# Kernel optimization log

Hardware: AMD Instinct MI355X
Metric: run time of the kernel (lower is better)

The kernel has to match this reference:

```python
import jax, jax.numpy as jnp
import numpy as np

SEL = 20   # selection_length
NN2 = 10   # org_dim*num_library_fns % SEL
NN3 = 22   # org_dim*num_library_fns // SEL - NN2


def _all_combos(L):
    # all 2^L binary vectors of length L; equals union over popcounts of
    # set(itertools.permutations([1]*c + [0]*(L-c))) in the torch code
    ints = jnp.arange(2 ** L, dtype=jnp.uint32)
    bits = (ints[:, None] >> jnp.arange(L, dtype=jnp.uint32)[None, :]) & jnp.uint32(1)
    return bits.astype(jnp.float32)  # [2^L, L]


def _chunk_step(params, combos, combo_sums, prob, chunk):
    """Replicates Model._compute_selarr_output_grad for one chunk.
    params: (W1 [H,L+1], b1 [H], W2 [1,H], b2 [1]) of net2 or net3.
    combos: [N, L] all binary vectors; combo_sums: [N] int popcounts.
    prob: scalar carry probability; chunk: [L] the actual selection.
    """
    W1, b1, W2, b2 = params
    N = combos.shape[0]
    x_all = jnp.concatenate([jnp.full((N, 1), prob, combos.dtype), combos], axis=1)  # [N, L+1]
    h = jnp.tanh(x_all @ W1.T + b1)          # [N, H]
    out = h @ W2[0] + b2[0]                  # [N]
    choices = jnp.round(jnp.sum(chunk)).astype(jnp.int32)
    mask = (combo_sums == choices).astype(combos.dtype)  # valid combinations only
    output_sum = jnp.sum(mask * jnp.exp(out))
    # grad_sum = sum_j out_j * d out_j / d theta (masked), closed form:
    w = mask * out
    s = (1.0 - h * h) * W2[0]                # [N, H]
    gs_W1 = jnp.einsum('n,nh,nd->hd', w, s, x_all)
    gs_b1 = jnp.einsum('n,nh->h', w, s)
    gs_W2 = jnp.einsum('n,nh->h', w, h)[None, :]
    gs_b2 = jnp.sum(w)[None]
    # the key combination = the actual chunk
    xk = jnp.concatenate([prob[None], chunk])
    hk = jnp.tanh(W1 @ xk + b1)
    outk = W2[0] @ hk + b2[0]
    sk = (1.0 - hk * hk) * W2[0]
    p_out = jnp.exp(outk) / output_sum
    grads = (jnp.outer(sk, xk) - gs_W1 / output_sum,
             sk - gs_b1 / output_sum,
             hk[None, :] - gs_W2 / output_sum,
             jnp.ones((1,), xk.dtype) - gs_b2 / output_sum)
    return p_out, grads


def _run_group(params, chunks, prob0):
    L = chunks.shape[1]
    combos = _all_combos(L)
    combo_sums = jnp.round(jnp.sum(combos, axis=1)).astype(jnp.int32)

    def step(carry, chunk):
        prob, acc = carry
        p, g = _chunk_step(params, combos, combo_sums, prob, chunk)
        acc = tuple(a + gi for a, gi in zip(acc, g))
        return (p, acc), p

    acc0 = tuple(jnp.zeros_like(p) for p in params)
    (prob_f, acc), ps = jax.lax.scan(step, (prob0, acc0), chunks)
    return prob_f, acc, ps


def setup_inputs() -> dict:
    key = jax.random.key(0)
    ks = jax.random.split(key, 10)
    total = NN2 * (SEL + 1) + NN3 * SEL  # 650
    selection_arr = jax.random.bernoulli(ks[0], 0.5, (total,)).astype(jnp.float32)
    p0 = jax.random.uniform(ks[1], (1,), jnp.float32)

    def lin(kw, kb, fan_out, fan_in):
        bound = 1.0 / np.sqrt(fan_in)
        W = jax.random.uniform(kw, (fan_out, fan_in), jnp.float32, -bound, bound)
        b = jax.random.uniform(kb, (fan_out,), jnp.float32, -bound, bound)
        return W, b

    W1_2, b1_2 = lin(ks[2], ks[3], 4, SEL + 2)  # net2: Linear(sel+2, 4)
    W2_2, b2_2 = lin(ks[4], ks[5], 1, 4)
    W1_3, b1_3 = lin(ks[6], ks[7], 4, SEL + 1)  # net3: Linear(sel+1, 4)
    W2_3, b2_3 = lin(ks[8], ks[9], 1, 4)
    return {'probability_lib_selection': p0, 'selection_arr': selection_arr,
            'W1_2': W1_2, 'b1_2': b1_2, 'W2_2': W2_2, 'b2_2': b2_2,
            'W1_3': W1_3, 'b1_3': b1_3, 'W2_3': W2_3, 'b2_3': b2_3}


def reference(probability_lib_selection, selection_arr,
              W1_2, b1_2, W2_2, b2_2, W1_3, b1_3, W2_3, b2_3):
    p0 = probability_lib_selection[0]
    n2 = NN2 * (SEL + 1)
    chunks2 = selection_arr[:n2].reshape(NN2, SEL + 1)
    chunks3 = selection_arr[n2:n2 + NN3 * SEL].reshape(NN3, SEL)
    p_after2, g2, ps2 = _run_group((W1_2, b1_2, W2_2, b2_2), chunks2, p0)
    _, g3, ps3 = _run_group((W1_3, b1_3, W2_3, b2_3), chunks3, p_after2)
    sample_probability_array = jnp.concatenate([p0[None], ps2, ps3])  # [1+NN2+NN3]
    return (sample_probability_array,) + g2 + g3
```

## Files before the change

### kernel.cpp

```cpp
#include <hip/hip_runtime.h>
#include <cstdint>
#include <cmath>

#define DEV __device__ __forceinline__

constexpr int SEL = 20;
constexpr int NSTEP2 = 10, NSTEP3 = 22, NSTEPS = 32;
constexpr int L2 = SEL + 1;
constexpr int L3 = SEL;
constexpr int FBE = 7;
constexpr int FBS2 = L2 - FBE;
constexpr int FBS3 = L3 - FBE;
constexpr int BT = 128;

typedef float v2f __attribute__((ext_vector_type(2)));

constexpr float K2E = 2.8853900817779268f;
constexpr float KE  = 1.4426950408889634f;

struct Binom { unsigned v[22][22]; };
constexpr Binom make_binom() {
  Binom b{};
  for (int n = 0; n < 22; n++) {
    b.v[n][0] = 1;
    for (int k = 1; k < 22; k++)
      b.v[n][k] = (k > n) ? 0u : (k == n ? 1u : b.v[n - 1][k - 1] + b.v[n - 1][k]);
  }
  return b;
}
constexpr Binom BN_H = make_binom();
__device__ constexpr Binom BN = make_binom();

constexpr unsigned ceil64u(unsigned x) { return (x + 63u) & ~63u; }
constexpr int padded_count(int NB) {
  int s = 0;
  for (int k = 0; k <= NB; k++) s += (int)ceil64u(BN_H.v[NB][k]);
  return s;
}
constexpr int NPAT2P = padded_count(FBS2);
constexpr int NPAT3P = padded_count(FBS3);

constexpr int SUMS_STRIDE = 96;
constexpr int OFF_SUMS   = 0;
constexpr int OFF_KEYB   = OFF_SUMS + NSTEPS * SUMS_STRIDE;
constexpr int OFF_CT     = OFF_KEYB + 128;
constexpr int OFF_CB     = OFF_CT + 32;
constexpr int OFF_REP    = OFF_CB + 32;
constexpr int OFF_ZEND   = OFF_REP + 32;
constexpr int OFF_PAT2   = OFF_ZEND;
constexpr int OFF_PAT3   = OFF_PAT2 + NPAT2P;

DEV float fast_tanh(float x) {
  float e = exp2f(x * K2E);
  return 1.0f - 2.0f * __builtin_amdgcn_rcpf(e + 1.0f);
}
DEV float fast_exp(float x) { return exp2f(x * KE); }
DEV void gatomic(float* p, float v) { unsafeAtomicAdd(p, v); }

DEV unsigned gosper(unsigned cmb) {
  unsigned u = cmb & (~cmb + 1u);
  unsigned v = cmb + u;
  return v | ((cmb ^ v) >> (1 + __ffs(u)));
}

DEV float dppsum64(float x) {
  float f = x;
  f += __int_as_float(__builtin_amdgcn_update_dpp(0, __float_as_int(f), 0x111, 0xf, 0xf, false));
  f += __int_as_float(__builtin_amdgcn_update_dpp(0, __float_as_int(f), 0x112, 0xf, 0xf, false));
  f += __int_as_float(__builtin_amdgcn_update_dpp(0, __float_as_int(f), 0x114, 0xf, 0xf, false));
  f += __int_as_float(__builtin_amdgcn_update_dpp(0, __float_as_int(f), 0x118, 0xf, 0xf, false));
  f += __int_as_float(__builtin_amdgcn_update_dpp(0, __float_as_int(f), 0x142, 0xa, 0xf, false));
  f += __int_as_float(__builtin_amdgcn_update_dpp(0, __float_as_int(f), 0x143, 0xc, 0xf, false));
  return f;
}

__global__ void kz(const float* p0, const float* sel,
                   const float* W1_2, const float* b1_2,
                   const float* W1_3, const float* b1_3, float* ws) {
  int tx = threadIdx.x;
  if (blockIdx.x == 0) {
    __shared__ int sc[NSTEPS];
    for (int i = tx; i < OFF_ZEND; i += blockDim.x) ws[i] = 0.0f;
    __syncthreads();
    if (tx < NSTEPS) {
      int t = tx;
      int g = (t < NSTEP2) ? 0 : 1;
      int L = g ? L3 : L2;
      const float* sbase = sel + (g ? (NSTEP2 * L2 + (t - NSTEP2) * L3) : t * L2);
      unsigned cb = 0; int c = 0;
      for (int d = 0; d < L; d++)
        if (sbase[d] > 0.5f) { cb |= 1u << d; c++; }
      sc[t] = c;
      ((int*)ws)[OFF_CT + t] = c;
      ((unsigned*)ws)[OFF_CB + t] = cb;
      const float* W1 = g ? W1_3 : W1_2;
      const float* b1 = g ? b1_3 : b1_2;
      for (int h = 0; h < 4; h++) {
        float s = b1[h];
        for (int d = 0; d < L; d++)
          if ((cb >> d) & 1) s += W1[h * (L + 1) + 1 + d];
        ws[OFF_KEYB + t * 4 + h] = s;
      }
    }
    __syncthreads();
    if (tx < NSTEPS) {
      int r = tx;
      int start = (tx == 0) ? 0 : ((tx < NSTEP2) ? 1 : NSTEP2);
      for (int u = start; u < tx; u++)
        if (sc[u] == sc[tx]) { r = u; break; }
      ((int*)ws)[OFF_REP + tx] = r;
    }
  } else {
    int r = (blockIdx.x - 1) * 256 + tx;
    if (r >= NPAT2P + NPAT3P) return;
    int NB, rr, off;
    if (r < NPAT2P) { NB = FBS2; rr = r; off = OFF_PAT2; }
    else            { NB = FBS3; rr = r - NPAT2P; off = OFF_PAT3; }
    unsigned pat = 0xFFFFFFFFu;
    unsigned base = 0;
    for (int kk = 0; kk <= NB; kk++) {
      unsigned csz = BN.v[NB][kk];
      unsigned psz = (csz + 63u) & ~63u;
      if ((unsigned)rr < base + psz) {
        unsigned local = (unsigned)rr - base;
        if (local < csz) {
          unsigned p2 = 0; int k2 = kk;
          for (int bb = NB - 1; bb >= 0 && k2 > 0; bb--) {
            unsigned cnt = BN.v[bb][k2];
            if (local >= cnt) { p2 |= 1u << bb; local -= cnt; k2--; }
          }
          pat = p2;
        }
        break;
      }
      base += psz;
    }
    ((unsigned*)ws)[off + rr] = pat;
  }
}

template<int LL>
DEV void build_tabs(const float* W1, float4 add,
                    float4* tabEX, float4* tabS0, float4* tabS1) {
  constexpr int NS1 = 1 << (LL - 14);
  int tx = threadIdx.x;
  for (int i = tx; i < 256 + NS1; i += BT) {
    if (i < 128) {
      int e = i;
      float s0 = 0, s1 = 0, s2 = 0, s3 = 0;
      for (int j = 0; j < 7; j++) if ((e >> j) & 1) {
        s0 += W1[0 * (LL + 1) + 1 + j]; s1 += W1[1 * (LL + 1) + 1 + j];
        s2 += W1[2 * (LL + 1) + 1 + j]; s3 += W1[3 * (LL + 1) + 1 + j];
      }
      tabEX[e] = make_float4(exp2f(K2E * s0), exp2f(K2E * s1), exp2f(K2E * s2), exp2f(K2E * s3));
    } else if (i < 256) {
      int e = i - 128;
      float s0 = add.x, s1 = add.y, s2 = add.z, s3 = add.w;
      for (int j = 0; j < 7; j++) if ((e >> j) & 1) {
        s0 += W1[0 * (LL + 1) + 1 + 7 + j]; s1 += W1[1 * (LL + 1) + 1 + 7 + j];
        s2 += W1[2 * (LL + 1) + 1 + 7 + j]; s3 += W1[3 * (LL + 1) + 1 + 7 + j];
      }
      tabS0[e] = make_float4(s0, s1, s2, s3);
    } else {
      int e = i - 256;
      float s0 = 0, s1 = 0, s2 = 0, s3 = 0;
      for (int j = 0; j < LL - 14; j++) if ((e >> j) & 1) {
        s0 += W1[0 * (LL + 1) + 1 + 14 + j]; s1 += W1[1 * (LL + 1) + 1 + 14 + j];
        s2 += W1[2 * (LL + 1) + 1 + 14 + j]; s3 += W1[3 * (LL + 1) + 1 + 14 + j];
      }
      tabS1[e] = make_float4(s0, s1, s2, s3);
    }
  }
}

constexpr int KC_B2 = NPAT2P / BT;
constexpr int KC_B3 = NPAT3P / BT;
constexpr int KC_BLOCKS = NSTEP2 * KC_B2 + NSTEP3 * KC_B3;

template<int LL>
DEV void kc_work(int t, int sub, float pval,
                 const float* W1, const float* b1, const float* W2, const float* b2,
                 float* ws, float4* tabEX, float4* tabS0, float4* tabS1, float* sS) {
  constexpr int FS = LL - FBE;
  constexpr int NS1M = (1 << (LL - 14)) - 1;
  int tx = threadIdx.x;
  int c = ((const int*)ws)[OFF_CT + t];
  const unsigned* pats = ((const unsigned*)ws) + (LL == 21 ? OFF_PAT2 : OFF_PAT3);
  int pcF = __popc(pats[sub * BT]);
  int pcL = __popc(pats[sub * BT + 64]);
  if (c < pcF || c - pcL > FBE) return;
  float4 add = make_float4(b1[0] + pval * W1[0 * (LL + 1)], b1[1] + pval * W1[1 * (LL + 1)],
                           b1[2] + pval * W1[2 * (LL + 1)], b1[3] + pval * W1[3 * (LL + 1)]);
  build_tabs<LL>(W1, add, tabEX, tabS0, tabS1);
  if (tx < SUMS_STRIDE) sS[tx] = 0.0f;
  __syncthreads();
  unsigned pat = pats[sub * BT + tx];
  int ce = c - __popc(pat);
  int ce_s = __builtin_amdgcn_readfirstlane(ce);
  int trip = (ce_s >= 0 && ce_s <= FBE) ? (int)BN.v[FBE][ce_s] : 0;
  if (trip > 0) {
    float valid = (ce == ce_s) ? 1.0f : 0.0f;
    float4 vS0 = tabS0[pat & 127];
    float4 vS1 = tabS1[(pat >> 7) & NS1M];
    float E0 = exp2f(K2E * (vS0.x + vS1.x));
    float E1 = exp2f(K2E * (vS0.y + vS1.y));
    float E2 = exp2f(K2E * (vS0.z + vS1.z));
    float E3 = exp2f(K2E * (vS0.w + vS1.w));
    float w0 = W2[0], w1 = W2[1], w2 = W2[2], w3 = W2[3];
    float W0 = b2[0] + w0 + w1 + w2 + w3;
    float m0 = -2.0f * w0, m1 = -2.0f * w1, m2 = -2.0f * w2, m3 = -2.0f * w3;
    float M0 = 4.0f * w0, M1 = 4.0f * w1, M2 = 4.0f * w2, M3 = 4.0f * w3;

    float aE = 0.0f, aW = 0.0f;
    v2f aQa = {0, 0}, aQb = {0, 0}, ORa = {0, 0}, ORb = {0, 0};
#define G_DECL(k) v2f g##k##a = {0, 0}, g##k##b = {0, 0};
    G_DECL(0) G_DECL(1) G_DECL(2) G_DECL(3) G_DECL(4) G_DECL(5) G_DECL(6)
#undef G_DECL

    unsigned ivs = (1u << ce_s) - 1u;
    float4 tE = tabEX[ivs & 127];
#pragma unroll 1
    for (int k = 0; k < trip; k++) {
      float4 cur = tE;
      unsigned ivc = ivs;
      ivs = gosper(ivs);
      tE = tabEX[ivs & 127];
      float r0 = __builtin_amdgcn_rcpf(fmaf(cur.x, E0, 1.0f));
      float r1 = __builtin_amdgcn_rcpf(fmaf(cur.y, E1, 1.0f));
      float r2 = __builtin_amdgcn_rcpf(fmaf(cur.z, E2, 1.0f));
      float r3 = __builtin_amdgcn_rcpf(fmaf(cur.w, E3, 1.0f));
      float outv = W0;
      outv = fmaf(m0, r0, outv); outv = fmaf(m1, r1, outv);
      outv = fmaf(m2, r2, outv); outv = fmaf(m3, r3, outv);
      float e = exp2f(KE * outv) * valid;
      outv *= valid;
      float u0 = fmaf(-r0, r0, r0), u1 = fmaf(-r1, r1, r1);
      float u2 = fmaf(-r2, r2, r2), u3 = fmaf(-r3, r3, r3);
      float q0 = outv * (M0 * u0), q1 = outv * (M1 * u1);
      float q2 = outv * (M2 * u2), q3 = outv * (M3 * u3);
      v2f qa = {q0, q1}, qb = {q2, q3};
      aE += e; aW += outv;
      aQa += qa; aQb += qb;
      ORa += (v2f){outv * r0, outv * r1};
      ORb += (v2f){outv * r2, outv * r3};
#define G_UPD(k) if (ivc & (1u << k)) { g##k##a += qa; g##k##b += qb; }
      G_UPD(0) G_UPD(1) G_UPD(2) G_UPD(3) G_UPD(4) G_UPD(5) G_UPD(6)
#undef G_UPD
    }
    v2f aWHa = {aW - 2.0f * ORa.x, aW - 2.0f * ORa.y};
    v2f aWHb = {aW - 2.0f * ORb.x, aW - 2.0f * ORb.y};

    int lane = tx & 63;
    float rr;
    rr = dppsum64(aE); if (lane == 63 && rr != 0.0f) atomicAdd(&sS[0], rr);
    rr = dppsum64(aW); if (lane == 63 && rr != 0.0f) atomicAdd(&sS[1], rr);
    rr = dppsum64(aQa.x); if (lane == 63 && rr != 0.0f) atomicAdd(&sS[2], rr);
    rr = dppsum64(aQa.y); if (lane == 63 && rr != 0.0f) atomicAdd(&sS[3], rr);
    rr = dppsum64(aQb.x); if (lane == 63 && rr != 0.0f) atomicAdd(&sS[4], rr);
    rr = dppsum64(aQb.y); if (lane == 63 && rr != 0.0f) atomicAdd(&sS[5], rr);
    rr = dppsum64(aWHa.x); if (lane == 63 && rr != 0.0f) atomicAdd(&sS[6], rr);
    rr = dppsum64(aWHa.y); if (lane == 63 && rr != 0.0f) atomicAdd(&sS[7], rr);
    rr = dppsum64(aWHb.x); if (lane == 63 && rr != 0.0f) atomicAdd(&sS[8], rr);
    rr = dppsum64(aWHb.y); if (lane == 63 && rr != 0.0f) atomicAdd(&sS[9], rr);
#define GF(k) { \
    rr = dppsum64(g##k##a.x); if (lane == 63 && rr != 0.0f) atomicAdd(&sS[10 + 0 * 21 + k], rr); \
    rr = dppsum64(g##k##a.y); if (lane == 63 && rr != 0.0f) atomicAdd(&sS[10 + 1 * 21 + k], rr); \
    rr = dppsum64(g##k##b.x); if (lane == 63 && rr != 0.0f) atomicAdd(&sS[10 + 2 * 21 + k], rr); \
    rr = dppsum64(g##k##b.y); if (lane == 63 && rr != 0.0f) atomicAdd(&sS[10 + 3 * 21 + k], rr); }
    GF(0) GF(1) GF(2) GF(3) GF(4) GF(5) GF(6)
#undef GF
#pragma unroll
    for (int j = 0; j < 14; j++) {
      if (j < FS) {
        float m = (float)((pat >> j) & 1u);
        rr = dppsum64(m * aQa.x); if (lane == 63 && rr != 0.0f) atomicAdd(&sS[10 + 0 * 21 + FBE + j], rr);
        rr = dppsum64(m * aQa.y); if (lane == 63 && rr != 0.0f) atomicAdd(&sS[10 + 1 * 21 + FBE + j], rr);
        rr = dppsum64(m * aQb.x); if (lane == 63 && rr != 0.0f) atomicAdd(&sS[10 + 2 * 21 + FBE + j], rr);
        rr = dppsum64(m * aQb.y); if (lane == 63 && rr != 0.0f) atomicAdd(&sS[10 + 3 * 21 + FBE + j], rr);
      }
    }
  }
  __syncthreads();
  if (tx < SUMS_STRIDE) {
    float v = sS[tx];
    if (v != 0.0f) gatomic(&ws[OFF_SUMS + t * SUMS_STRIDE + tx], v);
  }
}

__global__ __launch_bounds__(BT) void kc(
    const float* p0,
    const float* W1_2, const float* b1_2, const float* W2_2, const float* b2_2,
    const float* W1_3, const float* b1_3, const float* W2_3, const float* b2_3,
    float* ws) {
  __shared__ float4 tabEX[128], tabS0[128], tabS1[128];
  __shared__ float sS[SUMS_STRIDE];
  int b = blockIdx.x;
  int t, sub;
  if (b < NSTEP2 * KC_B2) { t = b / KC_B2; sub = b % KC_B2; }
  else { int b3 = b - NSTEP2 * KC_B2; t = NSTEP2 + b3 / KC_B3; sub = b3 % KC_B3; }
  int rep = ((const int*)ws)[OFF_REP + t];
  if (rep != t) return;
  float pval = (t == 0) ? p0[0] : 0.0f;
  if (t < NSTEP2) kc_work<21>(t, sub, pval, W1_2, b1_2, W2_2, b2_2, ws, tabEX, tabS0, tabS1, sS);
  else            kc_work<20>(t, sub, pval, W1_3, b1_3, W2_3, b2_3, ws, tabEX, tabS0, tabS1, sS);
}

__global__ __launch_bounds__(256) void kd(const float* p0in,
                   const float* W1_2, const float* b1_2, const float* W2_2, const float* b2_2,
                   const float* W1_3, const float* b1_3, const float* W2_3, const float* b2_3,
                   const float* ws, float* out) {
  __shared__ float sS[NSTEPS * SUMS_STRIDE];
  __shared__ float sKEYB[128];
  __shared__ float sk_s[NSTEPS][4], hk_s[NSTEPS][4], pp_s[NSTEPS], s0i_s[NSTEPS];
  __shared__ int sREP[NSTEPS];
  int tx = threadIdx.x;
  for (int i = tx; i < NSTEPS * SUMS_STRIDE; i += 256) sS[i] = ws[OFF_SUMS + i];
  for (int i = tx; i < 128; i += 256) sKEYB[i] = ws[OFF_KEYB + i];
  if (tx < NSTEPS) sREP[tx] = ((const int*)ws)[OFF_REP + tx];
  __syncthreads();
  if (tx == 0) {
    float p = p0in[0];
    out[0] = p;
    for (int t = 0; t < NSTEPS; t++) {
      int g = (t < NSTEP2) ? 0 : 1;
      int L = g ? L3 : L2;
      const float* W1 = g ? W1_3 : W1_2;
      const float* W2 = g ? W2_3 : W2_2;
      float b2s = (g ? b2_3 : b2_2)[0];
      pp_s[t] = p;
      float outk = b2s;
      for (int h = 0; h < 4; h++)
        outk += W2[h] * fast_tanh(sKEYB[t * 4 + h] + p * W1[h * (L + 1)]);
      float Se = sS[sREP[t] * SUMS_STRIDE + 0];
      p = fast_exp(outk) / Se;
      out[1 + t] = p;
    }
  }
  __syncthreads();
  if (tx < NSTEPS) {
    int t = tx; int g = (t < NSTEP2) ? 0 : 1; int L = g ? L3 : L2;
    const float* W1 = g ? W1_3 : W1_2;
    const float* W2 = g ? W2_3 : W2_2;
    float p = pp_s[t];
    s0i_s[t] = 1.0f / sS[sREP[t] * SUMS_STRIDE + 0];
    for (int h = 0; h < 4; h++) {
      float hk = fast_tanh(sKEYB[t * 4 + h] + p * W1[h * (L + 1)]);
      hk_s[t][h] = hk;
      sk_s[t][h] = (1.0f - hk * hk) * W2[h];
    }
  }
  __syncthreads();
  const unsigned* cbp = (const unsigned*)ws;
  for (int o = 33 + tx; o < 223; o += blockDim.x) {
    float val = 0.0f;
    if (o < 130) {
      if (o < 121) {
        int e = o - 33; int h = e / 22, d = e % 22;
        for (int t = 0; t < NSTEP2; t++) {
          int rp = sREP[t];
          float xk = (d == 0) ? pp_s[t] : (float)((cbp[OFF_CB + t] >> (d - 1)) & 1);
          float gs = (d == 0) ? pp_s[t] * sS[rp * SUMS_STRIDE + 2 + h]
                              : sS[rp * SUMS_STRIDE + 10 + h * 21 + (d - 1)];
          val += sk_s[t][h] * xk - gs * s0i_s[t];
        }
      } else if (o < 125) { int h = o - 121;
        for (int t = 0; t < NSTEP2; t++) val += sk_s[t][h] - sS[sREP[t] * SUMS_STRIDE + 2 + h] * s0i_s[t];
      } else if (o < 129) { int h = o - 125;
        for (int t = 0; t < NSTEP2; t++) val += hk_s[t][h] - sS[sREP[t] * SUMS_STRIDE + 6 + h] * s0i_s[t];
      } else {
        for (int t = 0; t < NSTEP2; t++) val += 1.0f - sS[sREP[t] * SUMS_STRIDE + 1] * s0i_s[t];
      }
    } else {
      if (o < 214) {
        int e = o - 130; int h = e / 21, d = e % 21;
        for (int t = NSTEP2; t < NSTEPS; t++) {
          int rp = sREP[t];
          float xk = (d == 0) ? pp_s[t] : (float)((cbp[OFF_CB + t] >> (d - 1)) & 1);
          float gs = (d == 0) ? pp_s[t] * sS[rp * SUMS_STRIDE + 2 + h]
                              : sS[rp * SUMS_STRIDE + 10 + h * 21 + (d - 1)];
          val += sk_s[t][h] * xk - gs * s0i_s[t];
        }
      } else if (o < 218) { int h = o - 214;
        for (int t = NSTEP2; t < NSTEPS; t++) val += sk_s[t][h] - sS[sREP[t] * SUMS_STRIDE + 2 + h] * s0i_s[t];
      } else if (o < 222) { int h = o - 218;
        for (int t = NSTEP2; t < NSTEPS; t++) val += hk_s[t][h] - sS[sREP[t] * SUMS_STRIDE + 6 + h] * s0i_s[t];
      } else {
        for (int t = NSTEP2; t < NSTEPS; t++) val += 1.0f - sS[sREP[t] * SUMS_STRIDE + 1] * s0i_s[t];
      }
    }
    out[o] = val;
  }
}

extern "C" void kernel_launch(void* const* d_in, const int* in_sizes, int n_in,
                              void* d_out, int out_size, void* d_ws, size_t ws_size,
                              hipStream_t stream) {
  const float* p0   = (const float*)d_in[0];
  const float* sel  = (const float*)d_in[1];
  const float* W1_2 = (const float*)d_in[2]; const float* b1_2 = (const float*)d_in[3];
  const float* W2_2 = (const float*)d_in[4]; const float* b2_2 = (const float*)d_in[5];
  const float* W1_3 = (const float*)d_in[6]; const float* b1_3 = (const float*)d_in[7];
  const float* W2_3 = (const float*)d_in[8]; const float* b2_3 = (const float*)d_in[9];
  float* out = (float*)d_out;
  float* ws  = (float*)d_ws;
  hipLaunchKernelGGL(kz, dim3(1 + (NPAT2P + NPAT3P + 255) / 256), dim3(256), 0, stream,
                     p0, sel, W1_2, b1_2, W1_3, b1_3, ws);
  hipLaunchKernelGGL(kc, dim3(KC_BLOCKS), dim3(BT), 0, stream, p0,
                     W1_2, b1_2, W2_2, b2_2, W1_3, b1_3, W2_3, b2_3, ws);
  hipLaunchKernelGGL(kd, dim3(1), dim3(256), 0, stream, p0,
                     W1_2, b1_2, W2_2, b2_2, W1_3, b1_3, W2_3, b2_3, ws, out);
}
```

Baseline: 72.39 us.

## Precompute lookup tables once in setup kernel and use single-wave blocks

Per-block construction of the three lookup tables from W1 is moved into three dedicated blocks of the setup kernel, which write them to workspace once for each weight set (net2 with p0, net2 without, net3). The main kernel then only copies the tables into shared memory. Block size drops from 128 to 64 threads so each block is one wave, and per-block shared-memory reduction is replaced by direct global atomics from each wave. This removes redundant table building and block-level syncs, at the cost of more blocks, more global atomics, and one extra table read from global memory per block.

```diff
diff --git a/kernel.cpp b/kernel.cpp
--- a/kernel.cpp
+++ b/kernel.cpp
@@ -11,7 +11,7 @@
 constexpr int FBE = 7;
 constexpr int FBS2 = L2 - FBE;
 constexpr int FBS3 = L3 - FBE;
-constexpr int BT = 128;
+constexpr int BT = 64;
 
 typedef float v2f __attribute__((ext_vector_type(2)));
 
@@ -47,7 +47,8 @@
 constexpr int OFF_CB     = OFF_CT + 32;
 constexpr int OFF_REP    = OFF_CB + 32;
 constexpr int OFF_ZEND   = OFF_REP + 32;
-constexpr int OFF_PAT2   = OFF_ZEND;
+constexpr int OFF_TABS   = OFF_ZEND;
+constexpr int OFF_PAT2   = OFF_TABS + 3 * 384 * 4;
 constexpr int OFF_PAT3   = OFF_PAT2 + NPAT2P;
 
 DEV float fast_tanh(float x) {
@@ -78,7 +79,8 @@
                    const float* W1_2, const float* b1_2,
                    const float* W1_3, const float* b1_3, float* ws) {
   int tx = threadIdx.x;
-  if (blockIdx.x == 0) {
+  int b = blockIdx.x;
+  if (b == 0) {
     __shared__ int sc[NSTEPS];
     for (int i = tx; i < OFF_ZEND; i += blockDim.x) ws[i] = 0.0f;
     __syncthreads();
@@ -110,8 +112,43 @@
         if (sc[u] == sc[tx]) { r = u; break; }
       ((int*)ws)[OFF_REP + tx] = r;
     }
+  } else if (b <= 3) {
+    int set = b - 1;
+    int LL = (set < 2) ? L2 : L3;
+    const float* W1 = (set < 2) ? W1_2 : W1_3;
+    const float* b1 = (set < 2) ? b1_2 : b1_3;
+    float pval = (set == 0) ? p0[0] : 0.0f;
+    int NS1 = 1 << (LL - 14);
+    float4* gt = (float4*)(ws + OFF_TABS) + set * 384;
+    for (int i = tx; i < 256 + NS1; i += 256) {
+      float4 v;
+      float* vp = (float*)&v;
+      if (i < 128) {
+        int e = i;
+        for (int h = 0; h < 4; h++) {
+          float s = 0;
+          for (int j = 0; j < 7; j++) if ((e >> j) & 1) s += W1[h * (LL + 1) + 1 + j];
+          vp[h] = exp2f(K2E * s);
+        }
+      } else if (i < 256) {
+        int e = i - 128;
+        for (int h = 0; h < 4; h++) {
+          float s = b1[h] + pval * W1[h * (LL + 1)];
+          for (int j = 0; j < 7; j++) if ((e >> j) & 1) s += W1[h * (LL + 1) + 1 + 7 + j];
+          vp[h] = s;
+        }
+      } else {
+        int e = i - 256;
+        for (int h = 0; h < 4; h++) {
+          float s = 0;
+          for (int j = 0; j < LL - 14; j++) if ((e >> j) & 1) s += W1[h * (LL + 1) + 1 + 14 + j];
+          vp[h] = s;
+        }
+      }
+      gt[i] = v;
+    }
   } else {
-    int r = (blockIdx.x - 1) * 256 + tx;
+    int r = (b - 4) * 256 + tx;
     if (r >= NPAT2P + NPAT3P) return;
     int NB, rr, off;
     if (r < NPAT2P) { NB = FBS2; rr = r; off = OFF_PAT2; }
@@ -139,170 +176,132 @@
   }
 }
 
-template<int LL>
-DEV void build_tabs(const float* W1, float4 add,
-                    float4* tabEX, float4* tabS0, float4* tabS1) {
-  constexpr int NS1 = 1 << (LL - 14);
-  int tx = threadIdx.x;
-  for (int i = tx; i < 256 + NS1; i += BT) {
-    if (i < 128) {
-      int e = i;
-      float s0 = 0, s1 = 0, s2 = 0, s3 = 0;
-      for (int j = 0; j < 7; j++) if ((e >> j) & 1) {
-        s0 += W1[0 * (LL + 1) + 1 + j]; s1 += W1[1 * (LL + 1) + 1 + j];
-        s2 += W1[2 * (LL + 1) + 1 + j]; s3 += W1[3 * (LL + 1) + 1 + j];
-      }
-      tabEX[e] = make_float4(exp2f(K2E * s0), exp2f(K2E * s1), exp2f(K2E * s2), exp2f(K2E * s3));
-    } else if (i < 256) {
-      int e = i - 128;
-      float s0 = add.x, s1 = add.y, s2 = add.z, s3 = add.w;
-      for (int j = 0; j < 7; j++) if ((e >> j) & 1) {
-        s0 += W1[0 * (LL + 1) + 1 + 7 + j]; s1 += W1[1 * (LL + 1) + 1 + 7 + j];
-        s2 += W1[2 * (LL + 1) + 1 + 7 + j]; s3 += W1[3 * (LL + 1) + 1 + 7 + j];
-      }
-      tabS0[e] = make_float4(s0, s1, s2, s3);
-    } else {
-      int e = i - 256;
-      float s0 = 0, s1 = 0, s2 = 0, s3 = 0;
-      for (int j = 0; j < LL - 14; j++) if ((e >> j) & 1) {
-        s0 += W1[0 * (LL + 1) + 1 + 14 + j]; s1 += W1[1 * (LL + 1) + 1 + 14 + j];
-        s2 += W1[2 * (LL + 1) + 1 + 14 + j]; s3 += W1[3 * (LL + 1) + 1 + 14 + j];
-      }
-      tabS1[e] = make_float4(s0, s1, s2, s3);
-    }
-  }
-}
-
 constexpr int KC_B2 = NPAT2P / BT;
 constexpr int KC_B3 = NPAT3P / BT;
 constexpr int KC_BLOCKS = NSTEP2 * KC_B2 + NSTEP3 * KC_B3;
 
 template<int LL>
-DEV void kc_work(int t, int sub, float pval,
-                 const float* W1, const float* b1, const float* W2, const float* b2,
-                 float* ws, float4* tabEX, float4* tabS0, float4* tabS1, float* sS) {
+DEV void kc_work(int t, int sub, int set,
+                 const float* W2, const float* b2,
+                 float* ws, float4* tabL) {
   constexpr int FS = LL - FBE;
-  constexpr int NS1M = (1 << (LL - 14)) - 1;
+  constexpr int NS1 = 1 << (LL - 14);
+  constexpr int NS1M = NS1 - 1;
   int tx = threadIdx.x;
   int c = ((const int*)ws)[OFF_CT + t];
   const unsigned* pats = ((const unsigned*)ws) + (LL == 21 ? OFF_PAT2 : OFF_PAT3);
-  int pcF = __popc(pats[sub * BT]);
-  int pcL = __popc(pats[sub * BT + 64]);
-  if (c < pcF || c - pcL > FBE) return;
-  float4 add = make_float4(b1[0] + pval * W1[0 * (LL + 1)], b1[1] + pval * W1[1 * (LL + 1)],
-                           b1[2] + pval * W1[2 * (LL + 1)], b1[3] + pval * W1[3 * (LL + 1)]);
-  build_tabs<LL>(W1, add, tabEX, tabS0, tabS1);
-  if (tx < SUMS_STRIDE) sS[tx] = 0.0f;
-  __syncthreads();
   unsigned pat = pats[sub * BT + tx];
   int ce = c - __popc(pat);
   int ce_s = __builtin_amdgcn_readfirstlane(ce);
-  int trip = (ce_s >= 0 && ce_s <= FBE) ? (int)BN.v[FBE][ce_s] : 0;
-  if (trip > 0) {
-    float valid = (ce == ce_s) ? 1.0f : 0.0f;
-    float4 vS0 = tabS0[pat & 127];
-    float4 vS1 = tabS1[(pat >> 7) & NS1M];
-    float E0 = exp2f(K2E * (vS0.x + vS1.x));
-    float E1 = exp2f(K2E * (vS0.y + vS1.y));
-    float E2 = exp2f(K2E * (vS0.z + vS1.z));
-    float E3 = exp2f(K2E * (vS0.w + vS1.w));
-    float w0 = W2[0], w1 = W2[1], w2 = W2[2], w3 = W2[3];
-    float W0 = b2[0] + w0 + w1 + w2 + w3;
-    float m0 = -2.0f * w0, m1 = -2.0f * w1, m2 = -2.0f * w2, m3 = -2.0f * w3;
-    float M0 = 4.0f * w0, M1 = 4.0f * w1, M2 = 4.0f * w2, M3 = 4.0f * w3;
-
-    float aE = 0.0f, aW = 0.0f;
-    v2f aQa = {0, 0}, aQb = {0, 0}, ORa = {0, 0}, ORb = {0, 0};
+  if (ce_s < 0 || ce_s > FBE) return;
+  int trip = (int)BN.v[FBE][ce_s];
+  const float4* gt = (const float4*)(ws + OFF_TABS) + set * 384;
+  for (int i = tx; i < 256 + NS1; i += BT) tabL[i] = gt[i];
+  __syncthreads();
+  const float4* tabEX = tabL;
+  const float4* tabS0 = tabL + 128;
+  const float4* tabS1 = tabL + 256;
+
+  float valid = (ce == ce_s) ? 1.0f : 0.0f;
+  float4 vS0 = tabS0[pat & 127];
+  float4 vS1 = tabS1[(pat >> 7) & NS1M];
+  float E0 = exp2f(K2E * (vS0.x + vS1.x));
+  float E1 = exp2f(K2E * (vS0.y + vS1.y));
+  float E2 = exp2f(K2E * (vS0.z + vS1.z));
+  float E3 = exp2f(K2E * (vS0.w + vS1.w));
+  float w0 = W2[0], w1 = W2[1], w2 = W2[2], w3 = W2[3];
+  float W0 = b2[0] + w0 + w1 + w2 + w3;
+  float m0 = -2.0f * w0, m1 = -2.0f * w1, m2 = -2.0f * w2, m3 = -2.0f * w3;
+  float M0 = 4.0f * w0, M1 = 4.0f * w1, M2 = 4.0f * w2, M3 = 4.0f * w3;
+
+  float aE = 0.0f, aW = 0.0f;
+  v2f aQa = {0, 0}, aQb = {0, 0}, ORa = {0, 0}, ORb = {0, 0};
 #define G_DECL(k) v2f g##k##a = {0, 0}, g##k##b = {0, 0};
-    G_DECL(0) G_DECL(1) G_DECL(2) G_DECL(3) G_DECL(4) G_DECL(5) G_DECL(6)
+  G_DECL(0) G_DECL(1) G_DECL(2) G_DECL(3) G_DECL(4) G_DECL(5) G_DECL(6)
 #undef G_DECL
 
-    unsigned ivs = (1u << ce_s) - 1u;
-    float4 tE = tabEX[ivs & 127];
+  unsigned ivs = (1u << ce_s) - 1u;
+  float4 tE = tabEX[ivs & 127];
 #pragma unroll 1
-    for (int k = 0; k < trip; k++) {
-      float4 cur = tE;
-      unsigned ivc = ivs;
-      ivs = gosper(ivs);
-      tE = tabEX[ivs & 127];
-      float r0 = __builtin_amdgcn_rcpf(fmaf(cur.x, E0, 1.0f));
-      float r1 = __builtin_amdgcn_rcpf(fmaf(cur.y, E1, 1.0f));
-      float r2 = __builtin_amdgcn_rcpf(fmaf(cur.z, E2, 1.0f));
-      float r3 = __builtin_amdgcn_rcpf(fmaf(cur.w, E3, 1.0f));
-      float outv = W0;
-      outv = fmaf(m0, r0, outv); outv = fmaf(m1, r1, outv);
-      outv = fmaf(m2, r2, outv); outv = fmaf(m3, r3, outv);
-      float e = exp2f(KE * outv) * valid;
-      outv *= valid;
-      float u0 = fmaf(-r0, r0, r0), u1 = fmaf(-r1, r1, r1);
-      float u2 = fmaf(-r2, r2, r2), u3 = fmaf(-r3, r3, r3);
-      float q0 = outv * (M0 * u0), q1 = outv * (M1 * u1);
-      float q2 = outv * (M2 * u2), q3 = outv * (M3 * u3);
-      v2f qa = {q0, q1}, qb = {q2, q3};
-      aE += e; aW += outv;
-      aQa += qa; aQb += qb;
-      ORa += (v2f){outv * r0, outv * r1};
-      ORb += (v2f){outv * r2, outv * r3};
+  for (int k = 0; k < trip; k++) {
+    float4 cur = tE;
+    unsigned ivc = ivs;
+    ivs = gosper(ivs);
+    tE = tabEX[ivs & 127];
+    float r0 = __builtin_amdgcn_rcpf(fmaf(cur.x, E0, 1.0f));
+    float r1 = __builtin_amdgcn_rcpf(fmaf(cur.y, E1, 1.0f));
+    float r2 = __builtin_amdgcn_rcpf(fmaf(cur.z, E2, 1.0f));
+    float r3 = __builtin_amdgcn_rcpf(fmaf(cur.w, E3, 1.0f));
+    float outv = W0;
+    outv = fmaf(m0, r0, outv); outv = fmaf(m1, r1, outv);
+    outv = fmaf(m2, r2, outv); outv = fmaf(m3, r3, outv);
+    float e = exp2f(KE * outv) * valid;
+    outv *= valid;
+    float u0 = fmaf(-r0, r0, r0), u1 = fmaf(-r1, r1, r1);
+    float u2 = fmaf(-r2, r2, r2), u3 = fmaf(-r3, r3, r3);
+    float q0 = outv * (M0 * u0), q1 = outv * (M1 * u1);
+    float q2 = outv * (M2 * u2), q3 = outv * (M3 * u3);
+    v2f qa = {q0, q1}, qb = {q2, q3};
+    aE += e; aW += outv;
+    aQa += qa; aQb += qb;
+    ORa += (v2f){outv * r0, outv * r1};
+    ORb += (v2f){outv * r2, outv * r3};
 #define G_UPD(k) if (ivc & (1u << k)) { g##k##a += qa; g##k##b += qb; }
-      G_UPD(0) G_UPD(1) G_UPD(2) G_UPD(3) G_UPD(4) G_UPD(5) G_UPD(6)
+    G_UPD(0) G_UPD(1) G_UPD(2) G_UPD(3) G_UPD(4) G_UPD(5) G_UPD(6)
 #undef G_UPD
-    }
-    v2f aWHa = {aW - 2.0f * ORa.x, aW - 2.0f * ORa.y};
-    v2f aWHb = {aW - 2.0f * ORb.x, aW - 2.0f * ORb.y};
-
-    int lane = tx & 63;
-    float rr;
-    rr = dppsum64(aE); if (lane == 63 && rr != 0.0f) atomicAdd(&sS[0], rr);
-    rr = dppsum64(aW); if (lane == 63 && rr != 0.0f) atomicAdd(&sS[1], rr);
-    rr = dppsum64(aQa.x); if (lane == 63 && rr != 0.0f) atomicAdd(&sS[2], rr);
-    rr = dppsum64(aQa.y); if (lane == 63 && rr != 0.0f) atomicAdd(&sS[3], rr);
-    rr = dppsum64(aQb.x); if (lane == 63 && rr != 0.0f) atomicAdd(&sS[4], rr);
-    rr = dppsum64(aQb.y); if (lane == 63 && rr != 0.0f) atomicAdd(&sS[5], rr);
-    rr = dppsum64(aWHa.x); if (lane == 63 && rr != 0.0f) atomicAdd(&sS[6], rr);
-    rr = dppsum64(aWHa.y); if (lane == 63 && rr != 0.0f) atomicAdd(&sS[7], rr);
-    rr = dppsum64(aWHb.x); if (lane == 63 && rr != 0.0f) atomicAdd(&sS[8], rr);
-    rr = dppsum64(aWHb.y); if (lane == 63 && rr != 0.0f) atomicAdd(&sS[9], rr);
+  }
+  v2f aWHa = {aW - 2.0f * ORa.x, aW - 2.0f * ORa.y};
+  v2f aWHb = {aW - 2.0f * ORb.x, aW - 2.0f * ORb.y};
+
+  float* S = &ws[OFF_SUMS + t * SUMS_STRIDE];
+  int lane = tx;
+  float rr;
+  rr = dppsum64(aE); if (lane == 63 && rr != 0.0f) gatomic(&S[0], rr);
+  rr = dppsum64(aW); if (lane == 63 && rr != 0.0f) gatomic(&S[1], rr);
+  rr = dppsum64(aQa.x); if (lane == 63 && rr != 0.0f) gatomic(&S[2], rr);
+  rr = dppsum64(aQa.y); if (lane == 63 && rr != 0.0f) gatomic(&S[3], rr);
+  rr = dppsum64(aQb.x); if (lane == 63 && rr != 0.0f) gatomic(&S[4], rr);
+  rr = dppsum64(aQb.y); if (lane == 63 && rr != 0.0f) gatomic(&S[5], rr);
+  rr = dppsum64(aWHa.x); if (lane == 63 && rr != 0.0f) gatomic(&S[6], rr);
+  rr = dppsum64(aWHa.y); if (lane == 63 && rr != 0.0f) gatomic(&S[7], rr);
+  rr = dppsum64(aWHb.x); if (lane == 63 && rr != 0.0f) gatomic(&S[8], rr);
+  rr = dppsum64(aWHb.y); if (lane == 63 && rr != 0.0f) gatomic(&S[9], rr);
 #define GF(k) { \
-    rr = dppsum64(g##k##a.x); if (lane == 63 && rr != 0.0f) atomicAdd(&sS[10 + 0 * 21 + k], rr); \
-    rr = dppsum64(g##k##a.y); if (lane == 63 && rr != 0.0f) atomicAdd(&sS[10 + 1 * 21 + k], rr); \
-    rr = dppsum64(g##k##b.x); if (lane == 63 && rr != 0.0f) atomicAdd(&sS[10 + 2 * 21 + k], rr); \
-    rr = dppsum64(g##k##b.y); if (lane == 63 && rr != 0.0f) atomicAdd(&sS[10 + 3 * 21 + k], rr); }
-    GF(0) GF(1) GF(2) GF(3) GF(4) GF(5) GF(6)
+  rr = dppsum64(g##k##a.x); if (lane == 63 && rr != 0.0f) gatomic(&S[10 + 0 * 21 + k], rr); \
+  rr = dppsum64(g##k##a.y); if (lane == 63 && rr != 0.0f) gatomic(&S[10 + 1 * 21 + k], rr); \
+  rr = dppsum64(g##k##b.x); if (lane == 63 && rr != 0.0f) gatomic(&S[10 + 2 * 21 + k], rr); \
+  rr = dppsum64(g##k##b.y); if (lane == 63 && rr != 0.0f) gatomic(&S[10 + 3 * 21 + k], rr); }
+  GF(0) GF(1) GF(2) GF(3) GF(4) GF(5) GF(6)
 #undef GF
 #pragma unroll
-    for (int j = 0; j < 14; j++) {
-      if (j < FS) {
-        float m = (float)((pat >> j) & 1u);
-        rr = dppsum64(m * aQa.x); if (lane == 63 && rr != 0.0f) atomicAdd(&sS[10 + 0 * 21 + FBE + j], rr);
-        rr = dppsum64(m * aQa.y); if (lane == 63 && rr != 0.0f) atomicAdd(&sS[10 + 1 * 21 + FBE + j], rr);
-        rr = dppsum64(m * aQb.x); if (lane == 63 && rr != 0.0f) atomicAdd(&sS[10 + 2 * 21 + FBE + j], rr);
-        rr = dppsum64(m * aQb.y); if (lane == 63 && rr != 0.0f) atomicAdd(&sS[10 + 3 * 21 + FBE + j], rr);
-      }
-    }
-  }
-  __syncthreads();
-  if (tx < SUMS_STRIDE) {
-    float v = sS[tx];
-    if (v != 0.0f) gatomic(&ws[OFF_SUMS + t * SUMS_STRIDE + tx], v);
+  for (int j = 0; j < 14; j++) {
+    if (j < FS) {
+      float m = (float)((pat >> j) & 1u);
+      rr = dppsum64(m * aQa.x); if (lane == 63 && rr != 0.0f) gatomic(&S[10 + 0 * 21 + FBE + j], rr);
+      rr = dppsum64(m * aQa.y); if (lane == 63 && rr != 0.0f) gatomic(&S[10 + 1 * 21 + FBE + j], rr);
+      rr = dppsum64(m * aQb.x); if (lane == 63 && rr != 0.0f) gatomic(&S[10 + 2 * 21 + FBE + j], rr);
+      rr = dppsum64(m * aQb.y); if (lane == 63 && rr != 0.0f) gatomic(&S[10 + 3 * 21 + FBE + j], rr);
+    }
   }
 }
 
 __global__ __launch_bounds__(BT) void kc(
-    const float* p0,
-    const float* W1_2, const float* b1_2, const float* W2_2, const float* b2_2,
-    const float* W1_3, const float* b1_3, const float* W2_3, const float* b2_3,
+    const float* W2_2, const float* b2_2,
+    const float* W2_3, const float* b2_3,
     float* ws) {
-  __shared__ float4 tabEX[128], tabS0[128], tabS1[128];
-  __shared__ float sS[SUMS_STRIDE];
+  __shared__ float4 tabL[384];
   int b = blockIdx.x;
   int t, sub;
   if (b < NSTEP2 * KC_B2) { t = b / KC_B2; sub = b % KC_B2; }
   else { int b3 = b - NSTEP2 * KC_B2; t = NSTEP2 + b3 / KC_B3; sub = b3 % KC_B3; }
   int rep = ((const int*)ws)[OFF_REP + t];
   if (rep != t) return;
-  float pval = (t == 0) ? p0[0] : 0.0f;
-  if (t < NSTEP2) kc_work<21>(t, sub, pval, W1_2, b1_2, W2_2, b2_2, ws, tabEX, tabS0, tabS1, sS);
-  else            kc_work<20>(t, sub, pval, W1_3, b1_3, W2_3, b2_3, ws, tabEX, tabS0, tabS1, sS);
+  if (t < NSTEP2) {
+    int set = (t == 0) ? 0 : 1;
+    kc_work<21>(t, sub, set, W2_2, b2_2, ws, tabL);
+  } else {
+    kc_work<20>(t, sub, 2, W2_3, b2_3, ws, tabL);
+  }
 }
 
 __global__ __launch_bounds__(256) void kd(const float* p0in,
@@ -310,27 +309,30 @@
                    const float* W1_3, const float* b1_3, const float* W2_3, const float* b2_3,
                    const float* ws, float* out) {
   __shared__ float sS[NSTEPS * SUMS_STRIDE];
-  __shared__ float sKEYB[128];
+  __shared__ float sKEYB[128], sW1c0[8], sW2[8], sB2[2];
   __shared__ float sk_s[NSTEPS][4], hk_s[NSTEPS][4], pp_s[NSTEPS], s0i_s[NSTEPS];
   __shared__ int sREP[NSTEPS];
   int tx = threadIdx.x;
   for (int i = tx; i < NSTEPS * SUMS_STRIDE; i += 256) sS[i] = ws[OFF_SUMS + i];
   for (int i = tx; i < 128; i += 256) sKEYB[i] = ws[OFF_KEYB + i];
   if (tx < NSTEPS) sREP[tx] = ((const int*)ws)[OFF_REP + tx];
+  if (tx < 4) {
+    sW1c0[tx]     = W1_2[tx * (L2 + 1)];
+    sW1c0[4 + tx] = W1_3[tx * (L3 + 1)];
+    sW2[tx]     = W2_2[tx];
+    sW2[4 + tx] = W2_3[tx];
+  }
+  if (tx == 0) { sB2[0] = b2_2[0]; sB2[1] = b2_3[0]; }
   __syncthreads();
   if (tx == 0) {
     float p = p0in[0];
     out[0] = p;
     for (int t = 0; t < NSTEPS; t++) {
       int g = (t < NSTEP2) ? 0 : 1;
-      int L = g ? L3 : L2;
-      const float* W1 = g ? W1_3 : W1_2;
-      const float* W2 = g ? W2_3 : W2_2;
-      float b2s = (g ? b2_3 : b2_2)[0];
       pp_s[t] = p;
-      float outk = b2s;
+      float outk = sB2[g];
       for (int h = 0; h < 4; h++)
-        outk += W2[h] * fast_tanh(sKEYB[t * 4 + h] + p * W1[h * (L + 1)]);
+        outk += sW2[g * 4 + h] * fast_tanh(sKEYB[t * 4 + h] + p * sW1c0[g * 4 + h]);
       float Se = sS[sREP[t] * SUMS_STRIDE + 0];
       p = fast_exp(outk) / Se;
       out[1 + t] = p;
@@ -338,15 +340,13 @@
   }
   __syncthreads();
   if (tx < NSTEPS) {
-    int t = tx; int g = (t < NSTEP2) ? 0 : 1; int L = g ? L3 : L2;
-    const float* W1 = g ? W1_3 : W1_2;
-    const float* W2 = g ? W2_3 : W2_2;
+    int t = tx; int g = (t < NSTEP2) ? 0 : 1;
     float p = pp_s[t];
     s0i_s[t] = 1.0f / sS[sREP[t] * SUMS_STRIDE + 0];
     for (int h = 0; h < 4; h++) {
-      float hk = fast_tanh(sKEYB[t * 4 + h] + p * W1[h * (L + 1)]);
+      float hk = fast_tanh(sKEYB[t * 4 + h] + p * sW1c0[g * 4 + h]);
       hk_s[t][h] = hk;
-      sk_s[t][h] = (1.0f - hk * hk) * W2[h];
+      sk_s[t][h] = (1.0f - hk * hk) * sW2[g * 4 + h];
     }
   }
   __syncthreads();
@@ -403,10 +403,10 @@
   const float* W2_3 = (const float*)d_in[8]; const float* b2_3 = (const float*)d_in[9];
   float* out = (float*)d_out;
   float* ws  = (float*)d_ws;
-  hipLaunchKernelGGL(kz, dim3(1 + (NPAT2P + NPAT3P + 255) / 256), dim3(256), 0, stream,
+  hipLaunchKernelGGL(kz, dim3(4 + (NPAT2P + NPAT3P + 255) / 256), dim3(256), 0, stream,
                      p0, sel, W1_2, b1_2, W1_3, b1_3, ws);
-  hipLaunchKernelGGL(kc, dim3(KC_BLOCKS), dim3(BT), 0, stream, p0,
-                     W1_2, b1_2, W2_2, b2_2, W1_3, b1_3, W2_3, b2_3, ws);
+  hipLaunchKernelGGL(kc, dim3(KC_BLOCKS), dim3(BT), 0, stream,
+                     W2_2, b2_2, W2_3, b2_3, ws);
   hipLaunchKernelGGL(kd, dim3(1), dim3(256), 0, stream, p0,
                      W1_2, b1_2, W2_2, b2_2, W1_3, b1_3, W2_3, b2_3, ws, out);
 }
```

Result: slower. 139.8 us (+93.1%).
